# Kernel optimization log

Hardware: AMD Instinct MI355X
Metric: run time of the kernel (lower is better)

Reference implementation:

```python
import jax, jax.numpy as jnp
import numpy as np

HIDDEN = 4096
N_EXPERTS = 128
TOP_K = 8
N_GROUP = 1
TOPK_GROUP = 1
NORM_TOPK_PROB = True
ROUTED_SCALING = 1.0


def setup_inputs() -> dict:
    key = jax.random.key(0)
    k1, k2, k3 = jax.random.split(key, 3)
    hidden_states = jax.random.normal(k1, (4, 4096, HIDDEN), dtype=jnp.float32)
    weight = jax.random.normal(k2, (N_EXPERTS, HIDDEN), dtype=jnp.float32) * 0.02
    e_score_correction_bias = jax.random.normal(k3, (N_EXPERTS,), dtype=jnp.float32) * 0.02
    return {
        "hidden_states": hidden_states,
        "weight": weight,
        "e_score_correction_bias": e_score_correction_bias,
    }


def reference(hidden_states, weight, e_score_correction_bias):
    # flatten tokens: [T, H]
    h = hidden_states.reshape(-1, HIDDEN).astype(jnp.float32)
    # router logits -> sigmoid scores  [T, E]
    logits = jnp.einsum("th,eh->te", h, weight.astype(jnp.float32))
    scores = jax.nn.sigmoid(logits)
    scores_for_choice = scores + e_score_correction_bias[None, :]
    T = scores.shape[0]
    # group scores: sum of top-2 (bias-corrected) scores within each group  [T, G]
    grouped = scores_for_choice.reshape(T, N_GROUP, N_EXPERTS // N_GROUP)
    group_scores = jax.lax.top_k(grouped, 2)[0].sum(axis=-1)
    # select top groups, build expert mask  [T, E]
    group_idx = jax.lax.top_k(group_scores, TOPK_GROUP)[1]          # [T, topk_group]
    group_mask = jnp.zeros((T, N_GROUP), scores.dtype).at[
        jnp.arange(T)[:, None], group_idx].set(1.0)
    score_mask = jnp.repeat(group_mask, N_EXPERTS // N_GROUP, axis=1)
    masked_scores = jnp.where(score_mask > 0, scores_for_choice, 0.0)
    # final top-k experts over masked scores; weights gathered from raw scores
    topk_indices = jax.lax.top_k(masked_scores, TOP_K)[1]           # [T, top_k]
    topk_weights = jnp.take_along_axis(scores, topk_indices, axis=1)
    if NORM_TOPK_PROB:
        denom = topk_weights.sum(axis=-1, keepdims=True) + 1e-20
        topk_weights = topk_weights / denom
    topk_weights = topk_weights * ROUTED_SCALING
    return topk_indices, topk_weights
```

## Files before the change

kernel.cpp:

```cpp
#include <hip/hip_runtime.h>
#include <math.h>

#define HIDDEN 4096
#define NEXP   128
#define TOPK   8
#define BM     32
#define BKC    64
#define NCHUNK (HIDDEN / BKC)
#define SS     132

#define SMEM_USHORT 12288

typedef __attribute__((ext_vector_type(8))) short short8;
typedef __attribute__((ext_vector_type(4))) float f32x4;

__device__ __forceinline__ unsigned pack2(unsigned a, unsigned b) {
  return (a >> 16) | (b & 0xFFFF0000u);
}

struct Split3 { uint4 h, m, l; };
__device__ __forceinline__ Split3 split8(float4 a, float4 b) {
  float x[8] = {a.x, a.y, a.z, a.w, b.x, b.y, b.z, b.w};
  unsigned h[8], m[8], l[8];
#pragma unroll
  for (int j = 0; j < 8; ++j) {
    unsigned u  = __float_as_uint(x[j]);
    unsigned hb = (u + 0x8000u) & 0xFFFF0000u;
    float rh    = x[j] - __uint_as_float(hb);
    unsigned um = __float_as_uint(rh);
    unsigned mb = (um + 0x8000u) & 0xFFFF0000u;
    float rm    = rh - __uint_as_float(mb);
    h[j] = hb; m[j] = mb; l[j] = __float_as_uint(rm);
  }
  Split3 s;
  s.h = make_uint4(pack2(h[0],h[1]), pack2(h[2],h[3]), pack2(h[4],h[5]), pack2(h[6],h[7]));
  s.m = make_uint4(pack2(m[0],m[1]), pack2(m[2],m[3]), pack2(m[4],m[5]), pack2(m[6],m[7]));
  s.l = make_uint4(pack2(l[0],l[1]), pack2(l[2],l[3]), pack2(l[4],l[5]), pack2(l[6],l[7]));
  return s;
}

struct Split3x4 { uint2 h, m, l; };
__device__ __forceinline__ Split3x4 split4(float4 a) {
  float x[4] = {a.x, a.y, a.z, a.w};
  unsigned h[4], m[4], l[4];
#pragma unroll
  for (int j = 0; j < 4; ++j) {
    unsigned u  = __float_as_uint(x[j]);
    unsigned hb = (u + 0x8000u) & 0xFFFF0000u;
    float rh    = x[j] - __uint_as_float(hb);
    unsigned um = __float_as_uint(rh);
    unsigned mb = (um + 0x8000u) & 0xFFFF0000u;
    float rm    = rh - __uint_as_float(mb);
    h[j] = hb; m[j] = mb; l[j] = __float_as_uint(rm);
  }
  Split3x4 s;
  s.h = make_uint2(pack2(h[0],h[1]), pack2(h[2],h[3]));
  s.m = make_uint2(pack2(m[0],m[1]), pack2(m[2],m[3]));
  s.l = make_uint2(pack2(l[0],l[1]), pack2(l[2],l[3]));
  return s;
}

__global__ __launch_bounds__(256) void pack_w_kernel(
    const float* __restrict__ w, ushort* __restrict__ wp)
{
  const int g    = blockIdx.x * 256 + threadIdx.x;
  const int lane = g & 63;
  const int fid  = g >> 6;
  const int et   = fid >> 7;
  const int kc   = fid & 127;
  const int e    = et * 16 + (lane & 15);
  const int k0   = kc * 32 + (lane >> 4) * 8;
  const float4 x0 = *(const float4*)(w + (size_t)e * HIDDEN + k0);
  const float4 x1 = *(const float4*)(w + (size_t)e * HIDDEN + k0 + 4);
  Split3 s = split8(x0, x1);
  uint4* dst = (uint4*)wp + (size_t)fid * 3 * 64;
  dst[0 * 64 + lane] = s.h;
  dst[1 * 64 + lane] = s.m;
  dst[2 * 64 + lane] = s.l;
}

__global__ __launch_bounds__(512, 4) void router_kernel(
    const float*  __restrict__ h,
    const ushort* __restrict__ wp,
    const float*  __restrict__ bias,
    float* __restrict__ out,
    int T)
{
  __shared__ __align__(16) ushort smem_u[SMEM_USHORT];
  const int tid  = threadIdx.x;
  const int row0 = blockIdx.x * BM;

  const int wid  = tid >> 6;
  const int wn   = wid & 3;
  const int wk   = wid >> 2;
  const int lane = tid & 63;
  const int lrow = lane & 15;
  const int lk   = lane >> 4;

  const int sr = tid >> 4;
  const int sk = tid & 15;
  const float* gA = h + (size_t)(row0 + sr) * HIDDEN + sk * 4;
  const int six   = (sr * 64 + sk * 4) ^ ((sr & 7) << 3);

  f32x4 acc[2][2];
#pragma unroll
  for (int i = 0; i < 2; ++i)
#pragma unroll
    for (int j = 0; j < 2; ++j) acc[i][j] = (f32x4){0.f, 0.f, 0.f, 0.f};

  float4 pa = *(const float4*)(gA);

  for (int c = 0; c < NCHUNK; ++c) {
    const int kc = c * 2 + wk;
    short8 bf[2][3];
#pragma unroll
    for (int ni = 0; ni < 2; ++ni) {
      const size_t fb = (size_t)((wn * 2 + ni) * 128 + kc) * 1536 + lane * 8;
#pragma unroll
      for (int s = 0; s < 3; ++s)
        bf[ni][s] = *(const short8*)(wp + fb + s * 512);
    }

    const int b    = c & 1;
    const int abuf = b * 6144;
    {
      Split3x4 s = split4(pa);
      *(uint2*)(smem_u + abuf +    0 + six) = s.h;
      *(uint2*)(smem_u + abuf + 2048 + six) = s.m;
      *(uint2*)(smem_u + abuf + 4096 + six) = s.l;
    }
    if (c + 1 < NCHUNK) pa = *(const float4*)(gA + (c + 1) * BKC);
    __syncthreads();

    short8 af[2][3];
#pragma unroll
    for (int mi = 0; mi < 2; ++mi) {
      const int r  = mi * 16 + lrow;
      const int ix = (r * 64 + wk * 32 + lk * 8) ^ ((r & 7) << 3);
      af[mi][0] = *(const short8*)(smem_u + abuf +    0 + ix);
      af[mi][1] = *(const short8*)(smem_u + abuf + 2048 + ix);
      af[mi][2] = *(const short8*)(smem_u + abuf + 4096 + ix);
    }
#pragma unroll
    for (int mi = 0; mi < 2; ++mi)
#pragma unroll
      for (int ni = 0; ni < 2; ++ni) {
        f32x4 cc = acc[mi][ni];
        cc = __builtin_amdgcn_mfma_f32_16x16x32_bf16(af[mi][0], bf[ni][0], cc, 0, 0, 0);
        cc = __builtin_amdgcn_mfma_f32_16x16x32_bf16(af[mi][0], bf[ni][1], cc, 0, 0, 0);
        cc = __builtin_amdgcn_mfma_f32_16x16x32_bf16(af[mi][1], bf[ni][0], cc, 0, 0, 0);
        cc = __builtin_amdgcn_mfma_f32_16x16x32_bf16(af[mi][0], bf[ni][2], cc, 0, 0, 0);
        cc = __builtin_amdgcn_mfma_f32_16x16x32_bf16(af[mi][2], bf[ni][0], cc, 0, 0, 0);
        cc = __builtin_amdgcn_mfma_f32_16x16x32_bf16(af[mi][1], bf[ni][1], cc, 0, 0, 0);
        acc[mi][ni] = cc;
      }
  }

  __syncthreads();
  float* Ss = (float*)smem_u;
  if (wk == 1) {
#pragma unroll
    for (int mi = 0; mi < 2; ++mi)
#pragma unroll
      for (int ni = 0; ni < 2; ++ni)
#pragma unroll
        for (int j = 0; j < 4; ++j)
          Ss[(mi * 16 + lk * 4 + j) * SS + wn * 32 + ni * 16 + lrow] = acc[mi][ni][j];
  }
  __syncthreads();
  if (wk == 0) {
#pragma unroll
    for (int mi = 0; mi < 2; ++mi)
#pragma unroll
      for (int ni = 0; ni < 2; ++ni)
#pragma unroll
        for (int j = 0; j < 4; ++j) {
          const int ixs = (mi * 16 + lk * 4 + j) * SS + wn * 32 + ni * 16 + lrow;
          Ss[ixs] += acc[mi][ni][j];
        }
  }
  __syncthreads();

  const float bb0 = bias[lane];
  const float bb1 = bias[lane + 64];

  for (int t = wid; t < BM; t += 8) {
    const float lg0 = Ss[t * SS + lane];
    const float lg1 = Ss[t * SS + 64 + lane];
    const float s0 = 1.0f / (1.0f + expf(-lg0));
    const float s1 = 1.0f / (1.0f + expf(-lg1));
    float c0 = s0 + bb0;
    float c1 = s1 + bb1;

    int   sel_i[TOPK];
    float sel_r[TOPK];
    float rsum = 0.0f;
#pragma unroll
    for (int j = 0; j < TOPK; ++j) {
      const bool take0 = (c0 >= c1);
      float v  = take0 ? c0 : c1;
      float rr = take0 ? s0 : s1;
      int   ii = take0 ? lane : lane + 64;
#pragma unroll
      for (int off = 32; off > 0; off >>= 1) {
        const float ov  = __shfl_xor(v, off, 64);
        const float orr = __shfl_xor(rr, off, 64);
        const int   oi  = __shfl_xor(ii, off, 64);
        if (ov > v || (ov == v && oi < ii)) { v = ov; rr = orr; ii = oi; }
      }
      sel_i[j] = ii;
      sel_r[j] = rr;
      rsum += rr;
      if (ii == lane)      c0 = -__builtin_inff();
      if (ii == lane + 64) c1 = -__builtin_inff();
    }
    if (lane == 0) {
      const float inv = 1.0f / (rsum + 1e-20f);
      const size_t tok = (size_t)(row0 + t);
#pragma unroll
      for (int j = 0; j < TOPK; ++j) {
        out[tok * TOPK + j]                    = (float)sel_i[j];
        out[(size_t)T * TOPK + tok * TOPK + j] = sel_r[j] * inv;
      }
    }
  }
}

extern "C" void kernel_launch(void* const* d_in, const int* in_sizes, int n_in,
                              void* d_out, int out_size, void* d_ws, size_t ws_size,
                              hipStream_t stream) {
  const float* h    = (const float*)d_in[0];
  const float* w    = (const float*)d_in[1];
  const float* bias = (const float*)d_in[2];
  float* out = (float*)d_out;
  ushort* wp = (ushort*)d_ws;
  const int T = in_sizes[0] / HIDDEN;

  hipLaunchKernelGGL(pack_w_kernel, dim3(256), dim3(256), 0, stream, w, wp);

  dim3 grid(T / BM);
  dim3 block(512);
  hipLaunchKernelGGL(router_kernel, grid, block, 0, stream, h, wp, bias, out, T);
}
```

Baseline: 448.7 us.

## Software-pipeline router GEMM with register double-buffered B and one barrier per chunk

Restructures the main loop so that the A tile for the next chunk is split and staged into the alternate LDS buffer while the current chunk's MFMAs run. B fragments are double-buffered in registers and prefetched one chunk ahead, with a single lgkmcnt-wait plus raw barrier per chunk. Wave priority is raised around the MFMA block. This aims to hide global load and LDS staging latency behind compute, at the cost of more registers, which may lower occupancy under the 512x4 launch bound.

New measurement: 447.9 us. No clear change (-0.2%).

```diff
diff --git a/kernel.cpp b/kernel.cpp
--- a/kernel.cpp
+++ b/kernel.cpp
@@ -102,59 +102,94 @@
   const float* gA = h + (size_t)(row0 + sr) * HIDDEN + sk * 4;
   const int six   = (sr * 64 + sk * 4) ^ ((sr & 7) << 3);
 
+  int aix[2];
+#pragma unroll
+  for (int mi = 0; mi < 2; ++mi) {
+    const int r = mi * 16 + lrow;
+    aix[mi] = (r * 64 + wk * 32 + lk * 8) ^ ((r & 7) << 3);
+  }
+
+  const ushort* pB0 = wp + (size_t)((wn * 2 + 0) * 128 + wk) * 1536 + lane * 8;
+  const ushort* pB1 = wp + (size_t)((wn * 2 + 1) * 128 + wk) * 1536 + lane * 8;
+
   f32x4 acc[2][2];
 #pragma unroll
   for (int i = 0; i < 2; ++i)
 #pragma unroll
     for (int j = 0; j < 2; ++j) acc[i][j] = (f32x4){0.f, 0.f, 0.f, 0.f};
 
+  short8 bfA[2][3], bfB[2][3];
+
   float4 pa = *(const float4*)(gA);
-
-  for (int c = 0; c < NCHUNK; ++c) {
-    const int kc = c * 2 + wk;
-    short8 bf[2][3];
-#pragma unroll
-    for (int ni = 0; ni < 2; ++ni) {
-      const size_t fb = (size_t)((wn * 2 + ni) * 128 + kc) * 1536 + lane * 8;
-#pragma unroll
-      for (int s = 0; s < 3; ++s)
-        bf[ni][s] = *(const short8*)(wp + fb + s * 512);
-    }
-
-    const int b    = c & 1;
-    const int abuf = b * 6144;
-    {
+  {
+    Split3x4 s = split4(pa);
+    *(uint2*)(smem_u +    0 + six) = s.h;
+    *(uint2*)(smem_u + 2048 + six) = s.m;
+    *(uint2*)(smem_u + 4096 + six) = s.l;
+  }
+  pa = *(const float4*)(gA + BKC);
+  const float* gA2 = gA + 2 * BKC;
+#pragma unroll
+  for (int s = 0; s < 3; ++s) {
+    bfA[0][s] = *(const short8*)(pB0 + s * 512);
+    bfA[1][s] = *(const short8*)(pB1 + s * 512);
+  }
+  asm volatile("s_waitcnt lgkmcnt(0)" ::: "memory");
+  __builtin_amdgcn_s_barrier();
+
+  auto body = [&](short8 (&bfC)[2][3], short8 (&bfN)[2][3],
+                  const int BR, const int BW,
+                  const bool prefB, const bool stageA, const bool prefA,
+                  const bool bar) {
+    short8 af[2][3];
+#pragma unroll
+    for (int mi = 0; mi < 2; ++mi) {
+      af[mi][0] = *(const short8*)(smem_u + BR +    0 + aix[mi]);
+      af[mi][1] = *(const short8*)(smem_u + BR + 2048 + aix[mi]);
+      af[mi][2] = *(const short8*)(smem_u + BR + 4096 + aix[mi]);
+    }
+    if (prefB) {
+      pB0 += 3072; pB1 += 3072;
+#pragma unroll
+      for (int s = 0; s < 3; ++s) {
+        bfN[0][s] = *(const short8*)(pB0 + s * 512);
+        bfN[1][s] = *(const short8*)(pB1 + s * 512);
+      }
+    }
+    if (stageA) {
       Split3x4 s = split4(pa);
-      *(uint2*)(smem_u + abuf +    0 + six) = s.h;
-      *(uint2*)(smem_u + abuf + 2048 + six) = s.m;
-      *(uint2*)(smem_u + abuf + 4096 + six) = s.l;
-    }
-    if (c + 1 < NCHUNK) pa = *(const float4*)(gA + (c + 1) * BKC);
-    __syncthreads();
-
-    short8 af[2][3];
-#pragma unroll
-    for (int mi = 0; mi < 2; ++mi) {
-      const int r  = mi * 16 + lrow;
-      const int ix = (r * 64 + wk * 32 + lk * 8) ^ ((r & 7) << 3);
-      af[mi][0] = *(const short8*)(smem_u + abuf +    0 + ix);
-      af[mi][1] = *(const short8*)(smem_u + abuf + 2048 + ix);
-      af[mi][2] = *(const short8*)(smem_u + abuf + 4096 + ix);
-    }
+      *(uint2*)(smem_u + BW +    0 + six) = s.h;
+      *(uint2*)(smem_u + BW + 2048 + six) = s.m;
+      *(uint2*)(smem_u + BW + 4096 + six) = s.l;
+    }
+    if (prefA) { pa = *(const float4*)(gA2); gA2 += BKC; }
+    __builtin_amdgcn_s_setprio(1);
 #pragma unroll
     for (int mi = 0; mi < 2; ++mi)
 #pragma unroll
       for (int ni = 0; ni < 2; ++ni) {
         f32x4 cc = acc[mi][ni];
-        cc = __builtin_amdgcn_mfma_f32_16x16x32_bf16(af[mi][0], bf[ni][0], cc, 0, 0, 0);
-        cc = __builtin_amdgcn_mfma_f32_16x16x32_bf16(af[mi][0], bf[ni][1], cc, 0, 0, 0);
-        cc = __builtin_amdgcn_mfma_f32_16x16x32_bf16(af[mi][1], bf[ni][0], cc, 0, 0, 0);
-        cc = __builtin_amdgcn_mfma_f32_16x16x32_bf16(af[mi][0], bf[ni][2], cc, 0, 0, 0);
-        cc = __builtin_amdgcn_mfma_f32_16x16x32_bf16(af[mi][2], bf[ni][0], cc, 0, 0, 0);
-        cc = __builtin_amdgcn_mfma_f32_16x16x32_bf16(af[mi][1], bf[ni][1], cc, 0, 0, 0);
+        cc = __builtin_amdgcn_mfma_f32_16x16x32_bf16(af[mi][0], bfC[ni][0], cc, 0, 0, 0);
+        cc = __builtin_amdgcn_mfma_f32_16x16x32_bf16(af[mi][0], bfC[ni][1], cc, 0, 0, 0);
+        cc = __builtin_amdgcn_mfma_f32_16x16x32_bf16(af[mi][1], bfC[ni][0], cc, 0, 0, 0);
+        cc = __builtin_amdgcn_mfma_f32_16x16x32_bf16(af[mi][0], bfC[ni][2], cc, 0, 0, 0);
+        cc = __builtin_amdgcn_mfma_f32_16x16x32_bf16(af[mi][2], bfC[ni][0], cc, 0, 0, 0);
+        cc = __builtin_amdgcn_mfma_f32_16x16x32_bf16(af[mi][1], bfC[ni][1], cc, 0, 0, 0);
         acc[mi][ni] = cc;
       }
-  }
+    __builtin_amdgcn_s_setprio(0);
+    if (bar) {
+      asm volatile("s_waitcnt lgkmcnt(0)" ::: "memory");
+      __builtin_amdgcn_s_barrier();
+    }
+  };
+
+  for (int c = 0; c < NCHUNK - 2; c += 2) {
+    body(bfA, bfB, 0,    6144, true, true, true, true);
+    body(bfB, bfA, 6144, 0,    true, true, true, true);
+  }
+  body(bfA, bfB, 0,    6144, true,  true,  false, true);
+  body(bfB, bfA, 6144, 0,    false, false, false, false);
 
   __syncthreads();
   float* Ss = (float*)smem_u;
```

## Load A fragments directly from global, dropping LDS staging and per-chunk barrier

Applied to the files above, without the earlier changes.

Each wave now loads its own A-fragment rows straight from global memory into registers and does the bf16 triple split in registers, so the shared-memory double buffer and the __syncthreads in every K-chunk are gone. Weight pointers are precomputed, the loop is unrolled by two, and MFMA sections are wrapped in s_setprio to favour the matrix issue. In exchange, A data is no longer shared through LDS: the four wn-waves each read the same rows redundantly (4x global/L2 traffic for A), and the split is recomputed per wave, with no explicit prefetch to hide load latency.

Measured after the change: 507.8 us. +13.2%, slower.

```diff
diff --git a/kernel.cpp b/kernel.cpp
--- a/kernel.cpp
+++ b/kernel.cpp
@@ -8,8 +8,6 @@
 #define BKC    64
 #define NCHUNK (HIDDEN / BKC)
 #define SS     132
-
-#define SMEM_USHORT 12288
 
 typedef __attribute__((ext_vector_type(8))) short short8;
 typedef __attribute__((ext_vector_type(4))) float f32x4;
@@ -36,27 +34,6 @@
   s.h = make_uint4(pack2(h[0],h[1]), pack2(h[2],h[3]), pack2(h[4],h[5]), pack2(h[6],h[7]));
   s.m = make_uint4(pack2(m[0],m[1]), pack2(m[2],m[3]), pack2(m[4],m[5]), pack2(m[6],m[7]));
   s.l = make_uint4(pack2(l[0],l[1]), pack2(l[2],l[3]), pack2(l[4],l[5]), pack2(l[6],l[7]));
-  return s;
-}
-
-struct Split3x4 { uint2 h, m, l; };
-__device__ __forceinline__ Split3x4 split4(float4 a) {
-  float x[4] = {a.x, a.y, a.z, a.w};
-  unsigned h[4], m[4], l[4];
-#pragma unroll
-  for (int j = 0; j < 4; ++j) {
-    unsigned u  = __float_as_uint(x[j]);
-    unsigned hb = (u + 0x8000u) & 0xFFFF0000u;
-    float rh    = x[j] - __uint_as_float(hb);
-    unsigned um = __float_as_uint(rh);
-    unsigned mb = (um + 0x8000u) & 0xFFFF0000u;
-    float rm    = rh - __uint_as_float(mb);
-    h[j] = hb; m[j] = mb; l[j] = __float_as_uint(rm);
-  }
-  Split3x4 s;
-  s.h = make_uint2(pack2(h[0],h[1]), pack2(h[2],h[3]));
-  s.m = make_uint2(pack2(m[0],m[1]), pack2(m[2],m[3]));
-  s.l = make_uint2(pack2(l[0],l[1]), pack2(l[2],l[3]));
   return s;
 }
 
@@ -86,7 +63,7 @@
     float* __restrict__ out,
     int T)
 {
-  __shared__ __align__(16) ushort smem_u[SMEM_USHORT];
+  __shared__ float Ss[BM * SS];
   const int tid  = threadIdx.x;
   const int row0 = blockIdx.x * BM;
 
@@ -97,10 +74,11 @@
   const int lrow = lane & 15;
   const int lk   = lane >> 4;
 
-  const int sr = tid >> 4;
-  const int sk = tid & 15;
-  const float* gA = h + (size_t)(row0 + sr) * HIDDEN + sk * 4;
-  const int six   = (sr * 64 + sk * 4) ^ ((sr & 7) << 3);
+  const float* pA0 = h + (size_t)(row0 + lrow) * HIDDEN + wk * 32 + lk * 8;
+  const float* pA1 = pA0 + (size_t)16 * HIDDEN;
+
+  const ushort* pB0 = wp + (size_t)((wn * 2 + 0) * 128 + wk) * 1536 + (size_t)lane * 8;
+  const ushort* pB1 = wp + (size_t)((wn * 2 + 1) * 128 + wk) * 1536 + (size_t)lane * 8;
 
   f32x4 acc[2][2];
 #pragma unroll
@@ -108,39 +86,28 @@
 #pragma unroll
     for (int j = 0; j < 2; ++j) acc[i][j] = (f32x4){0.f, 0.f, 0.f, 0.f};
 
-  float4 pa = *(const float4*)(gA);
-
+#pragma unroll 2
   for (int c = 0; c < NCHUNK; ++c) {
-    const int kc = c * 2 + wk;
     short8 bf[2][3];
-#pragma unroll
-    for (int ni = 0; ni < 2; ++ni) {
-      const size_t fb = (size_t)((wn * 2 + ni) * 128 + kc) * 1536 + lane * 8;
-#pragma unroll
-      for (int s = 0; s < 3; ++s)
-        bf[ni][s] = *(const short8*)(wp + fb + s * 512);
-    }
-
-    const int b    = c & 1;
-    const int abuf = b * 6144;
+    const ushort* b0 = pB0 + (size_t)c * 3072;
+    const ushort* b1 = pB1 + (size_t)c * 3072;
+#pragma unroll
+    for (int s = 0; s < 3; ++s) {
+      bf[0][s] = *(const short8*)(b0 + s * 512);
+      bf[1][s] = *(const short8*)(b1 + s * 512);
+    }
+    const float4 a00 = *(const float4*)(pA0 + c * BKC);
+    const float4 a01 = *(const float4*)(pA0 + c * BKC + 4);
+    const float4 a10 = *(const float4*)(pA1 + c * BKC);
+    const float4 a11 = *(const float4*)(pA1 + c * BKC + 4);
+    short8 af[2][3];
     {
-      Split3x4 s = split4(pa);
-      *(uint2*)(smem_u + abuf +    0 + six) = s.h;
-      *(uint2*)(smem_u + abuf + 2048 + six) = s.m;
-      *(uint2*)(smem_u + abuf + 4096 + six) = s.l;
-    }
-    if (c + 1 < NCHUNK) pa = *(const float4*)(gA + (c + 1) * BKC);
-    __syncthreads();
-
-    short8 af[2][3];
-#pragma unroll
-    for (int mi = 0; mi < 2; ++mi) {
-      const int r  = mi * 16 + lrow;
-      const int ix = (r * 64 + wk * 32 + lk * 8) ^ ((r & 7) << 3);
-      af[mi][0] = *(const short8*)(smem_u + abuf +    0 + ix);
-      af[mi][1] = *(const short8*)(smem_u + abuf + 2048 + ix);
-      af[mi][2] = *(const short8*)(smem_u + abuf + 4096 + ix);
-    }
+      Split3 s0 = split8(a00, a01);
+      af[0][0] = *(short8*)&s0.h; af[0][1] = *(short8*)&s0.m; af[0][2] = *(short8*)&s0.l;
+      Split3 s1 = split8(a10, a11);
+      af[1][0] = *(short8*)&s1.h; af[1][1] = *(short8*)&s1.m; af[1][2] = *(short8*)&s1.l;
+    }
+    __builtin_amdgcn_s_setprio(1);
 #pragma unroll
     for (int mi = 0; mi < 2; ++mi)
 #pragma unroll
@@ -154,10 +121,9 @@
         cc = __builtin_amdgcn_mfma_f32_16x16x32_bf16(af[mi][1], bf[ni][1], cc, 0, 0, 0);
         acc[mi][ni] = cc;
       }
-  }
-
-  __syncthreads();
-  float* Ss = (float*)smem_u;
+    __builtin_amdgcn_s_setprio(0);
+  }
+
   if (wk == 1) {
 #pragma unroll
     for (int mi = 0; mi < 2; ++mi)
```
